# Kernel optimization log

Hardware: AMD Instinct MI355X
Metric: run time of the kernel (lower is better)

Reference implementation:

```python
import jax, jax.numpy as jnp
import numpy as np

N_NODES = 100000
N_EDGES = 1600000
DK = 32
OUT_DIM = 32


def setup_inputs() -> dict:
    key = jax.random.key(0)
    ks = jax.random.split(key, 7)
    X = jax.random.normal(ks[0], (N_NODES, DK), dtype=jnp.float32)
    K = jax.random.normal(ks[1], (N_NODES, DK), dtype=jnp.float32)
    V = jax.random.normal(ks[2], (N_NODES, DK), dtype=jnp.float32)
    # output projection (nn.Dense(out_dim)) params
    W_o = jax.random.normal(ks[3], (DK, OUT_DIM), dtype=jnp.float32) / np.sqrt(DK)
    b_o = jnp.zeros((OUT_DIM,), dtype=jnp.float32)
    # sparsity descriptor td: edge list, dst sorted so segment ops see sorted ids
    src = jax.random.randint(ks[4], (N_EDGES,), 0, N_NODES, dtype=jnp.int32)
    dst = jnp.sort(jax.random.randint(ks[5], (N_EDGES,), 0, N_NODES, dtype=jnp.int32))
    return {"X": X, "K": K, "V": V, "W_o": W_o, "b_o": b_o,
            "src": src, "dst": dst, "num_seg": N_NODES}


def reference(X, K, V, W_o, b_o, src, dst, num_seg):
    dk = X.shape[-1]
    # per-edge attention logits: <Q[dst], K[src]> / dk  -> (E,)
    scores = jnp.einsum('ed,ed->e', jnp.take(X, dst, axis=0),
                        jnp.take(K, src, axis=0)) / dk
    # segment (per-neighborhood) softmax over edges sharing a dst node
    seg_max = jax.ops.segment_max(scores, dst, num_segments=num_seg,
                                  indices_are_sorted=True)
    e = jnp.exp(scores - jnp.take(seg_max, dst))
    denom = jax.ops.segment_sum(e, dst, num_segments=num_seg,
                                indices_are_sorted=True)
    alpha = e / jnp.take(denom, dst)  # (E,)
    # weighted aggregation of values, scattered back to nodes -> (N, dk)
    agg = jax.ops.segment_sum(alpha[:, None] * jnp.take(V, src, axis=0), dst,
                              num_segments=num_seg, indices_are_sorted=True)
    # output projection W_o
    return agg @ W_o + b_o
```

## Files before the change

### kernel.cpp

```cpp
#include <hip/hip_runtime.h>
#include <math.h>

#define DK 32
#define OUT_DIM 32

typedef float    f32x4 __attribute__((ext_vector_type(4)));
typedef _Float16 h2    __attribute__((ext_vector_type(2)));
typedef _Float16 h8    __attribute__((ext_vector_type(8)));

#if __has_builtin(__builtin_amdgcn_fdot2)
#define FDOT2(a, b, c) __builtin_amdgcn_fdot2((a), (b), (c), false)
#else
#define FDOT2(a, b, c) ((c) + (float)(a).x * (float)(b).x + (float)(a).y * (float)(b).y)
#endif

__device__ __forceinline__ h2 as_h2(unsigned u) {
    union { unsigned u; h2 h; } v; v.u = u; return v.h;
}
__device__ __forceinline__ unsigned as_u32(h2 h) {
    union { unsigned u; h2 h; } v; v.h = h; return v.u;
}
__device__ __forceinline__ h2 shfl_xor_h2(h2 v, int m) {
    union { unsigned u; h2 h; } x; x.h = v;
    x.u = (unsigned)__shfl_xor((int)x.u, m);
    return x.h;
}

__global__ void prep_kernel(const int* __restrict__ dst,
                            const float4* __restrict__ K4,
                            const float4* __restrict__ V4,
                            int E, int N,
                            int* __restrict__ row_ptr,
                            uint4* __restrict__ KVH) {
    const int t = blockIdx.x * blockDim.x + threadIdx.x;
    if (t < E) {
        const int cur  = dst[t];
        const int prev = (t == 0) ? -1 : dst[t - 1];
        for (int j = prev + 1; j <= cur; ++j) row_ptr[j] = t;
        if (t == E - 1) {
            for (int j = cur + 1; j <= N; ++j) row_ptr[j] = E;
        }
    }
    if (t < N * 8) {
        const float4 kf = K4[t];
        const float4 vf = V4[t];
        h2 k01, k23, v01, v23;
        k01.x = (_Float16)kf.x;  k01.y = (_Float16)kf.y;
        k23.x = (_Float16)kf.z;  k23.y = (_Float16)kf.w;
        v01.x = (_Float16)vf.x;  v01.y = (_Float16)vf.y;
        v23.x = (_Float16)vf.z;  v23.y = (_Float16)vf.w;
        uint4 o;
        o.x = as_u32(k01); o.y = as_u32(k23); o.z = as_u32(v01); o.w = as_u32(v23);
        KVH[t] = o;
    }
}

__global__ void build_row_ptr_kernel(const int* __restrict__ dst, int E, int N,
                                     int* __restrict__ row_ptr) {
    int e = blockIdx.x * blockDim.x + threadIdx.x;
    if (e >= E) return;
    int cur  = dst[e];
    int prev = (e == 0) ? -1 : dst[e - 1];
    for (int j = prev + 1; j <= cur; ++j) row_ptr[j] = e;
    if (e == E - 1) {
        for (int j = cur + 1; j <= N; ++j) row_ptr[j] = E;
    }
}

__global__ __launch_bounds__(256) void gat_fused_kernel(
    const float* __restrict__ X, const uint4* __restrict__ KV,
    const float* __restrict__ Wo, const float* __restrict__ bo,
    const int* __restrict__ src, const int* __restrict__ row_ptr,
    float* __restrict__ out, int N) {

    __shared__ uint4 s_part[16 * 17];

    const int tid  = threadIdx.x;
    const int w    = tid >> 6;
    const int lane = tid & 63;
    const int g    = lane >> 3;
    const int c    = lane & 7;

    const int n_blk = blockIdx.x * 16;
    const int n_w   = n_blk + w * 4;

    const int rpv = row_ptr[min(n_w + min(lane, 4), N)];

    const float4* X4 = (const float4*)X;
    unsigned* part32 = (unsigned*)s_part;
    const float scale = 0.03125f;

    for (int pr = 0; pr < 2; ++pr) {
        const int ia = pr * 2;
        const int beginA = __builtin_amdgcn_readlane(rpv, ia);
        const int endA   = __builtin_amdgcn_readlane(rpv, ia + 1);
        const int endB   = __builtin_amdgcn_readlane(rpv, ia + 2);
        const int beginB = endA;
        const int nA = n_w + ia;
        const int nB = nA + 1;

        float4 qa = X4[min(nA, N - 1) * 8 + c];
        float4 qb = X4[min(nB, N - 1) * 8 + c];
        h2 qa01, qa23, qb01, qb23;
        qa01.x = (_Float16)(qa.x * scale);  qa01.y = (_Float16)(qa.y * scale);
        qa23.x = (_Float16)(qa.z * scale);  qa23.y = (_Float16)(qa.w * scale);
        qb01.x = (_Float16)(qb.x * scale);  qb01.y = (_Float16)(qb.y * scale);
        qb23.x = (_Float16)(qb.z * scale);  qb23.y = (_Float16)(qb.w * scale);

        float lA = 0.0f, lB = 0.0f;
        h2 aA01 = (h2)0, aA23 = (h2)0, aB01 = (h2)0, aB23 = (h2)0;

        const int capA = max(endA - 1, 0);
        const int capB = max(endB - 1, 0);
        int eA = beginA, eB = beginB;

        auto step = [&](const uint4& A0, const uint4& A1,
                        const uint4& B0, const uint4& B1) {
            float p0 = FDOT2(as_h2(A0.y), qa23, FDOT2(as_h2(A0.x), qa01, 0.0f));
            float p1 = FDOT2(as_h2(A1.y), qa23, FDOT2(as_h2(A1.x), qa01, 0.0f));
            float p2 = FDOT2(as_h2(B0.y), qb23, FDOT2(as_h2(B0.x), qb01, 0.0f));
            float p3 = FDOT2(as_h2(B1.y), qb23, FDOT2(as_h2(B1.x), qb01, 0.0f));
            p0 += __shfl_xor(p0, 1);  p1 += __shfl_xor(p1, 1);
            p2 += __shfl_xor(p2, 1);  p3 += __shfl_xor(p3, 1);
            p0 += __shfl_xor(p0, 2);  p1 += __shfl_xor(p1, 2);
            p2 += __shfl_xor(p2, 2);  p3 += __shfl_xor(p3, 2);
            p0 += __shfl_xor(p0, 4);  p1 += __shfl_xor(p1, 4);
            p2 += __shfl_xor(p2, 4);  p3 += __shfl_xor(p3, 4);

            const float w0 = (eA + g     < endA) ? __expf(p0) : 0.0f;
            const float w1 = (eA + 8 + g < endA) ? __expf(p1) : 0.0f;
            const float w2 = (eB + g     < endB) ? __expf(p2) : 0.0f;
            const float w3 = (eB + 8 + g < endB) ? __expf(p3) : 0.0f;
            lA += w0 + w1;
            lB += w2 + w3;

            h2 wh0; wh0.x = (_Float16)w0; wh0.y = wh0.x;
            h2 wh1; wh1.x = (_Float16)w1; wh1.y = wh1.x;
            h2 wh2; wh2.x = (_Float16)w2; wh2.y = wh2.x;
            h2 wh3; wh3.x = (_Float16)w3; wh3.y = wh3.x;
            aA01 += wh0 * as_h2(A0.z);  aA23 += wh0 * as_h2(A0.w);
            aA01 += wh1 * as_h2(A1.z);  aA23 += wh1 * as_h2(A1.w);
            aB01 += wh2 * as_h2(B0.z);  aB23 += wh2 * as_h2(B0.w);
            aB01 += wh3 * as_h2(B1.z);  aB23 += wh3 * as_h2(B1.w);
        };

        if (eA < endA || eB < endB) {
            int sp0 = src[min(eA + g,     capA)];
            int sp1 = src[min(eA + 8 + g, capA)];
            int sp2 = src[min(eB + g,     capB)];
            int sp3 = src[min(eB + 8 + g, capB)];
            uint4 P0 = KV[sp0 * 8 + c];
            uint4 P1 = KV[sp1 * 8 + c];
            uint4 P2 = KV[sp2 * 8 + c];
            uint4 P3 = KV[sp3 * 8 + c];
            int sq0 = 0, sq1 = 0, sq2 = 0, sq3 = 0;
            uint4 Q0, Q1, Q2, Q3;
            bool more = (eA + 16 < endA) || (eB + 16 < endB);
            if (more) {
                sq0 = src[min(eA + 16 + g, capA)];
                sq1 = src[min(eA + 24 + g, capA)];
                sq2 = src[min(eB + 16 + g, capB)];
                sq3 = src[min(eB + 24 + g, capB)];
            }
            for (;;) {
                bool more2 = false;
                if (more) {
                    Q0 = KV[sq0 * 8 + c];
                    Q1 = KV[sq1 * 8 + c];
                    Q2 = KV[sq2 * 8 + c];
                    Q3 = KV[sq3 * 8 + c];
                    more2 = (eA + 32 < endA) || (eB + 32 < endB);
                    if (more2) {
                        sp0 = src[min(eA + 32 + g, capA)];
                        sp1 = src[min(eA + 40 + g, capA)];
                        sp2 = src[min(eB + 32 + g, capB)];
                        sp3 = src[min(eB + 40 + g, capB)];
                    }
                }
                step(P0, P1, P2, P3);
                eA += 16; eB += 16;
                if (!more) break;

                bool more3 = false;
                if (more2) {
                    P0 = KV[sp0 * 8 + c];
                    P1 = KV[sp1 * 8 + c];
                    P2 = KV[sp2 * 8 + c];
                    P3 = KV[sp3 * 8 + c];
                    more3 = (eA + 32 < endA) || (eB + 32 < endB);
                    if (more3) {
                        sq0 = src[min(eA + 32 + g, capA)];
                        sq1 = src[min(eA + 40 + g, capA)];
                        sq2 = src[min(eB + 32 + g, capB)];
                        sq3 = src[min(eB + 40 + g, capB)];
                    }
                }
                step(Q0, Q1, Q2, Q3);
                eA += 16; eB += 16;
                if (!more2) break;
                more = more3;
            }
        }

        lA   += __shfl_xor(lA, 8);
        aA01 += shfl_xor_h2(aA01, 8);
        aA23 += shfl_xor_h2(aA23, 8);
        lA += __shfl_xor(lA, 16);  lA += __shfl_xor(lA, 32);

        lB   += __shfl_xor(lB, 8);
        aB01 += shfl_xor_h2(aB01, 8);
        aB23 += shfl_xor_h2(aB23, 8);
        lB += __shfl_xor(lB, 16);  lB += __shfl_xor(lB, 32);

        const float invA = (endA > beginA) ? (1.0f / lA) : 0.0f;
        const float invB = (endB > beginB) ? (1.0f / lB) : 0.0f;
        h2 ivA; ivA.x = (_Float16)invA; ivA.y = ivA.x;
        h2 ivB; ivB.x = (_Float16)invB; ivB.y = ivB.x;
        aA01 *= ivA;  aA23 *= ivA;
        aB01 *= ivB;  aB23 *= ivB;

        if ((g & 1) == 0) {
            const int p   = g >> 1;
            const int row = w * 4 + ia;
            int off = row * 68 + p * 16 + c * 2;
            part32[off]     = as_u32(aA01);
            part32[off + 1] = as_u32(aA23);
            off += 68;
            part32[off]     = as_u32(aB01);
            part32[off + 1] = as_u32(aB23);
        }
    }

    __syncthreads();

    if (w == 0) {
        const int quad = lane >> 4;
        const int col  = lane & 15;

        union BF { h8 v; _Float16 u[8]; };
        BF bf0, bf1;
#pragma unroll
        for (int j2 = 0; j2 < 8; ++j2) {
            bf0.u[j2] = (_Float16)Wo[(quad * 8 + j2) * OUT_DIM + col];
            bf1.u[j2] = (_Float16)Wo[(quad * 8 + j2) * OUT_DIM + 16 + col];
        }
        const float bias0 = bo[col];
        const float bias1 = bo[16 + col];

        union AF { uint4 u; h8 v; };
        f32x4 C0 = {bias0, bias0, bias0, bias0};
        f32x4 C1 = {bias1, bias1, bias1, bias1};
#pragma unroll
        for (int cc = 0; cc < 4; ++cc) {
            AF a;
            a.u = s_part[col * 17 + cc * 4 + quad];
            C0 = __builtin_amdgcn_mfma_f32_16x16x32_f16(a.v, bf0.v, C0, 0, 0, 0);
            C1 = __builtin_amdgcn_mfma_f32_16x16x32_f16(a.v, bf1.v, C1, 0, 0, 0);
        }
#pragma unroll
        for (int r = 0; r < 4; ++r) {
            const int n = n_blk + quad * 4 + r;
            if (n < N) {
                out[n * OUT_DIM + col]      = C0[r];
                out[n * OUT_DIM + 16 + col] = C1[r];
            }
        }
    }
}

__global__ __launch_bounds__(256) void gat_node_f32_kernel(
    const float* __restrict__ X, const float* __restrict__ Km,
    const float* __restrict__ Vm, const float* __restrict__ Wo,
    const float* __restrict__ bo, const int* __restrict__ src,
    const int* __restrict__ row_ptr, float* __restrict__ out, int N) {
    const int tid  = threadIdx.x;
    const int wave = tid >> 6;
    const int lane = tid & 63;
    const int g    = lane >> 3;
    const int c    = lane & 7;
    const int j    = lane & 31;
    const int half = lane >> 5;
    const int n = blockIdx.x * 4 + wave;
    if (n >= N) return;
    const int begin = row_ptr[n];
    const int end   = row_ptr[n + 1];
    const float4* X4 = (const float4*)X;
    const float4* K4 = (const float4*)Km;
    const float4* V4 = (const float4*)Vm;
    const float4 q4 = X4[n * 8 + c];
    float  l   = 0.0f;
    float4 acc = make_float4(0.0f, 0.0f, 0.0f, 0.0f);
    for (int e0 = begin; e0 < end; e0 += 16) {
        const int  ea = e0 + g;
        const int  eb = ea + 8;
        const bool va = ea < end;
        const bool vb = eb < end;
        const int sa = src[min(ea, end - 1)];
        const int sb = src[min(eb, end - 1)];
        const float4 ka  = K4[sa * 8 + c];
        const float4 kb  = K4[sb * 8 + c];
        const float4 vva = V4[sa * 8 + c];
        const float4 vvb = V4[sb * 8 + c];
        float pa = fmaf(ka.x, q4.x, fmaf(ka.y, q4.y, fmaf(ka.z, q4.z, ka.w * q4.w)));
        float pb = fmaf(kb.x, q4.x, fmaf(kb.y, q4.y, fmaf(kb.z, q4.z, kb.w * q4.w)));
        pa += __shfl_xor(pa, 1);  pb += __shfl_xor(pb, 1);
        pa += __shfl_xor(pa, 2);  pb += __shfl_xor(pb, 2);
        pa += __shfl_xor(pa, 4);  pb += __shfl_xor(pb, 4);
        const float wa = va ? __expf(pa * 0.03125f) : 0.0f;
        const float wb = vb ? __expf(pb * 0.03125f) : 0.0f;
        l += wa + wb;
        acc.x = fmaf(wa, vva.x, acc.x);  acc.y = fmaf(wa, vva.y, acc.y);
        acc.z = fmaf(wa, vva.z, acc.z);  acc.w = fmaf(wa, vva.w, acc.w);
        acc.x = fmaf(wb, vvb.x, acc.x);  acc.y = fmaf(wb, vvb.y, acc.y);
        acc.z = fmaf(wb, vvb.z, acc.z);  acc.w = fmaf(wb, vvb.w, acc.w);
    }
#pragma unroll
    for (int m = 8; m <= 32; m <<= 1) {
        l     += __shfl_xor(l, m);
        acc.x += __shfl_xor(acc.x, m);
        acc.y += __shfl_xor(acc.y, m);
        acc.z += __shfl_xor(acc.z, m);
        acc.w += __shfl_xor(acc.w, m);
    }
    const float inv = (end > begin) ? (1.0f / l) : 0.0f;
    float ag[4] = {acc.x, acc.y, acc.z, acc.w};
    float s = 0.0f;
#pragma unroll
    for (int k = 0; k < 32; ++k) {
        const float a = __int_as_float(
            __builtin_amdgcn_readlane(__float_as_int(ag[k & 3]), k >> 2));
        s = fmaf(a, Wo[k * OUT_DIM + j], s);
    }
    if (half == 0) {
        out[n * OUT_DIM + j] = fmaf(s, inv, bo[j]);
    }
}

extern "C" void kernel_launch(void* const* d_in, const int* in_sizes, int n_in,
                              void* d_out, int out_size, void* d_ws, size_t ws_size,
                              hipStream_t stream) {
    const float* X  = (const float*)d_in[0];
    const float* Km = (const float*)d_in[1];
    const float* Vm = (const float*)d_in[2];
    const float* Wo = (const float*)d_in[3];
    const float* bo = (const float*)d_in[4];
    const int* src  = (const int*)d_in[5];
    const int* dst  = (const int*)d_in[6];

    const int N = in_sizes[0] / DK;
    const int E = in_sizes[5];

    int* row_ptr = (int*)d_ws;
    const size_t kv_off = (((size_t)(N + 1) * 4) + 127) & ~(size_t)127;
    unsigned* KV = (unsigned*)((char*)d_ws + kv_off);
    const size_t need = kv_off + (size_t)N * DK * 4;
    float* out = (float*)d_out;

    const int tb = 256;

    if (ws_size >= need) {
        const int total  = N * 8;
        const int prep_n = (E > total) ? E : total;
        prep_kernel<<<(prep_n + tb - 1) / tb, tb, 0, stream>>>(
            dst, (const float4*)Km, (const float4*)Vm, E, N,
            row_ptr, (uint4*)KV);
        const int grid = (N + 15) / 16;
        gat_fused_kernel<<<grid, 256, 0, stream>>>(X, (const uint4*)KV, Wo, bo,
                                                   src, row_ptr, out, N);
    } else {
        build_row_ptr_kernel<<<(E + tb - 1) / tb, tb, 0, stream>>>(dst, E, N, row_ptr);
        const int grid = (N + 3) / 4;
        gat_node_f32_kernel<<<grid, 256, 0, stream>>>(X, Km, Vm, Wo, bo,
                                                      src, row_ptr, out, N);
    }
}
```

Measured before the change: 133.1 us.

## Process four nodes per wave concurrently with triple-buffered gather pipeline and exp2

The fused attention kernel now handles all four nodes of a wave in one pass instead of two pairs. Each node gets one 8-edge slot per step, and KV gathers run through a three-deep software pipeline so more loads are in flight. The 1/ln2 factor is folded into the query scale so the softmax weight is computed with a native exp2 instead of expf. The prep kernel now loads four dst entries per thread with an int4 read, which shrinks the grid that builds row_ptr. The price is higher register pressure from the four-way state and triple buffers, and the prep change adds a serial loop per thread.

```diff
diff --git a/kernel.cpp b/kernel.cpp
--- a/kernel.cpp
+++ b/kernel.cpp
@@ -12,6 +12,12 @@
 #define FDOT2(a, b, c) __builtin_amdgcn_fdot2((a), (b), (c), false)
 #else
 #define FDOT2(a, b, c) ((c) + (float)(a).x * (float)(b).x + (float)(a).y * (float)(b).y)
+#endif
+
+#if __has_builtin(__builtin_amdgcn_exp2f)
+#define EXP2F(x) __builtin_amdgcn_exp2f(x)
+#else
+#define EXP2F(x) exp2f(x)
 #endif
 
 __device__ __forceinline__ h2 as_h2(unsigned u) {
@@ -32,13 +38,28 @@
                             int E, int N,
                             int* __restrict__ row_ptr,
                             uint4* __restrict__ KVH) {
-    const int t = blockIdx.x * blockDim.x + threadIdx.x;
-    if (t < E) {
-        const int cur  = dst[t];
-        const int prev = (t == 0) ? -1 : dst[t - 1];
-        for (int j = prev + 1; j <= cur; ++j) row_ptr[j] = t;
-        if (t == E - 1) {
-            for (int j = cur + 1; j <= N; ++j) row_ptr[j] = E;
+    const int t  = blockIdx.x * blockDim.x + threadIdx.x;
+    const int e0 = t * 4;
+    if (e0 < E) {
+        int cur[4];
+        if (e0 + 4 <= E) {
+            const int4 dd = *(const int4*)(dst + e0);
+            cur[0] = dd.x; cur[1] = dd.y; cur[2] = dd.z; cur[3] = dd.w;
+        } else {
+#pragma unroll
+            for (int k = 0; k < 4; ++k)
+                cur[k] = (e0 + k < E) ? dst[e0 + k] : 0;
+        }
+        int prev = (e0 == 0) ? -1 : dst[e0 - 1];
+#pragma unroll
+        for (int k = 0; k < 4; ++k) {
+            const int ee = e0 + k;
+            if (ee < E) {
+                for (int j = prev + 1; j <= cur[k]; ++j) row_ptr[j] = ee;
+                if (ee == E - 1)
+                    for (int j = cur[k] + 1; j <= N; ++j) row_ptr[j] = E;
+                prev = cur[k];
+            }
         }
     }
     if (t < N * 8) {
@@ -88,146 +109,118 @@
 
     const float4* X4 = (const float4*)X;
     unsigned* part32 = (unsigned*)s_part;
-    const float scale = 0.03125f;
-
-    for (int pr = 0; pr < 2; ++pr) {
-        const int ia = pr * 2;
-        const int beginA = __builtin_amdgcn_readlane(rpv, ia);
-        const int endA   = __builtin_amdgcn_readlane(rpv, ia + 1);
-        const int endB   = __builtin_amdgcn_readlane(rpv, ia + 2);
-        const int beginB = endA;
-        const int nA = n_w + ia;
-        const int nB = nA + 1;
-
-        float4 qa = X4[min(nA, N - 1) * 8 + c];
-        float4 qb = X4[min(nB, N - 1) * 8 + c];
-        h2 qa01, qa23, qb01, qb23;
-        qa01.x = (_Float16)(qa.x * scale);  qa01.y = (_Float16)(qa.y * scale);
-        qa23.x = (_Float16)(qa.z * scale);  qa23.y = (_Float16)(qa.w * scale);
-        qb01.x = (_Float16)(qb.x * scale);  qb01.y = (_Float16)(qb.y * scale);
-        qb23.x = (_Float16)(qb.z * scale);  qb23.y = (_Float16)(qb.w * scale);
-
-        float lA = 0.0f, lB = 0.0f;
-        h2 aA01 = (h2)0, aA23 = (h2)0, aB01 = (h2)0, aB23 = (h2)0;
-
-        const int capA = max(endA - 1, 0);
-        const int capB = max(endB - 1, 0);
-        int eA = beginA, eB = beginB;
-
-        auto step = [&](const uint4& A0, const uint4& A1,
-                        const uint4& B0, const uint4& B1) {
-            float p0 = FDOT2(as_h2(A0.y), qa23, FDOT2(as_h2(A0.x), qa01, 0.0f));
-            float p1 = FDOT2(as_h2(A1.y), qa23, FDOT2(as_h2(A1.x), qa01, 0.0f));
-            float p2 = FDOT2(as_h2(B0.y), qb23, FDOT2(as_h2(B0.x), qb01, 0.0f));
-            float p3 = FDOT2(as_h2(B1.y), qb23, FDOT2(as_h2(B1.x), qb01, 0.0f));
-            p0 += __shfl_xor(p0, 1);  p1 += __shfl_xor(p1, 1);
-            p2 += __shfl_xor(p2, 1);  p3 += __shfl_xor(p3, 1);
-            p0 += __shfl_xor(p0, 2);  p1 += __shfl_xor(p1, 2);
-            p2 += __shfl_xor(p2, 2);  p3 += __shfl_xor(p3, 2);
-            p0 += __shfl_xor(p0, 4);  p1 += __shfl_xor(p1, 4);
-            p2 += __shfl_xor(p2, 4);  p3 += __shfl_xor(p3, 4);
-
-            const float w0 = (eA + g     < endA) ? __expf(p0) : 0.0f;
-            const float w1 = (eA + 8 + g < endA) ? __expf(p1) : 0.0f;
-            const float w2 = (eB + g     < endB) ? __expf(p2) : 0.0f;
-            const float w3 = (eB + 8 + g < endB) ? __expf(p3) : 0.0f;
-            lA += w0 + w1;
-            lB += w2 + w3;
-
-            h2 wh0; wh0.x = (_Float16)w0; wh0.y = wh0.x;
-            h2 wh1; wh1.x = (_Float16)w1; wh1.y = wh1.x;
-            h2 wh2; wh2.x = (_Float16)w2; wh2.y = wh2.x;
-            h2 wh3; wh3.x = (_Float16)w3; wh3.y = wh3.x;
-            aA01 += wh0 * as_h2(A0.z);  aA23 += wh0 * as_h2(A0.w);
-            aA01 += wh1 * as_h2(A1.z);  aA23 += wh1 * as_h2(A1.w);
-            aB01 += wh2 * as_h2(B0.z);  aB23 += wh2 * as_h2(B0.w);
-            aB01 += wh3 * as_h2(B1.z);  aB23 += wh3 * as_h2(B1.w);
-        };
-
-        if (eA < endA || eB < endB) {
-            int sp0 = src[min(eA + g,     capA)];
-            int sp1 = src[min(eA + 8 + g, capA)];
-            int sp2 = src[min(eB + g,     capB)];
-            int sp3 = src[min(eB + 8 + g, capB)];
-            uint4 P0 = KV[sp0 * 8 + c];
-            uint4 P1 = KV[sp1 * 8 + c];
-            uint4 P2 = KV[sp2 * 8 + c];
-            uint4 P3 = KV[sp3 * 8 + c];
-            int sq0 = 0, sq1 = 0, sq2 = 0, sq3 = 0;
-            uint4 Q0, Q1, Q2, Q3;
-            bool more = (eA + 16 < endA) || (eB + 16 < endB);
-            if (more) {
-                sq0 = src[min(eA + 16 + g, capA)];
-                sq1 = src[min(eA + 24 + g, capA)];
-                sq2 = src[min(eB + 16 + g, capB)];
-                sq3 = src[min(eB + 24 + g, capB)];
-            }
-            for (;;) {
-                bool more2 = false;
-                if (more) {
-                    Q0 = KV[sq0 * 8 + c];
-                    Q1 = KV[sq1 * 8 + c];
-                    Q2 = KV[sq2 * 8 + c];
-                    Q3 = KV[sq3 * 8 + c];
-                    more2 = (eA + 32 < endA) || (eB + 32 < endB);
-                    if (more2) {
-                        sp0 = src[min(eA + 32 + g, capA)];
-                        sp1 = src[min(eA + 40 + g, capA)];
-                        sp2 = src[min(eB + 32 + g, capB)];
-                        sp3 = src[min(eB + 40 + g, capB)];
-                    }
-                }
-                step(P0, P1, P2, P3);
-                eA += 16; eB += 16;
-                if (!more) break;
-
-                bool more3 = false;
-                if (more2) {
-                    P0 = KV[sp0 * 8 + c];
-                    P1 = KV[sp1 * 8 + c];
-                    P2 = KV[sp2 * 8 + c];
-                    P3 = KV[sp3 * 8 + c];
-                    more3 = (eA + 32 < endA) || (eB + 32 < endB);
-                    if (more3) {
-                        sq0 = src[min(eA + 32 + g, capA)];
-                        sq1 = src[min(eA + 40 + g, capA)];
-                        sq2 = src[min(eB + 32 + g, capB)];
-                        sq3 = src[min(eB + 40 + g, capB)];
-                    }
-                }
-                step(Q0, Q1, Q2, Q3);
-                eA += 16; eB += 16;
-                if (!more2) break;
-                more = more3;
-            }
-        }
-
-        lA   += __shfl_xor(lA, 8);
-        aA01 += shfl_xor_h2(aA01, 8);
-        aA23 += shfl_xor_h2(aA23, 8);
-        lA += __shfl_xor(lA, 16);  lA += __shfl_xor(lA, 32);
-
-        lB   += __shfl_xor(lB, 8);
-        aB01 += shfl_xor_h2(aB01, 8);
-        aB23 += shfl_xor_h2(aB23, 8);
-        lB += __shfl_xor(lB, 16);  lB += __shfl_xor(lB, 32);
-
-        const float invA = (endA > beginA) ? (1.0f / lA) : 0.0f;
-        const float invB = (endB > beginB) ? (1.0f / lB) : 0.0f;
-        h2 ivA; ivA.x = (_Float16)invA; ivA.y = ivA.x;
-        h2 ivB; ivB.x = (_Float16)invB; ivB.y = ivB.x;
-        aA01 *= ivA;  aA23 *= ivA;
-        aB01 *= ivB;  aB23 *= ivB;
-
-        if ((g & 1) == 0) {
-            const int p   = g >> 1;
-            const int row = w * 4 + ia;
-            int off = row * 68 + p * 16 + c * 2;
-            part32[off]     = as_u32(aA01);
-            part32[off + 1] = as_u32(aA23);
-            off += 68;
-            part32[off]     = as_u32(aB01);
-            part32[off + 1] = as_u32(aB23);
+    const float scale = 0.03125f * 1.44269504f;
+
+    int beg[4], en[4], cap[4], e[4];
+#pragma unroll
+    for (int i = 0; i < 4; ++i) {
+        beg[i] = __builtin_amdgcn_readlane(rpv, i);
+        en[i]  = __builtin_amdgcn_readlane(rpv, i + 1);
+        cap[i] = max(en[i] - 1, 0);
+        e[i]   = beg[i];
+    }
+
+    h2 q01[4], q23[4];
+#pragma unroll
+    for (int i = 0; i < 4; ++i) {
+        const float4 qf = X4[min(n_w + i, N - 1) * 8 + c];
+        q01[i].x = (_Float16)(qf.x * scale);
+        q01[i].y = (_Float16)(qf.y * scale);
+        q23[i].x = (_Float16)(qf.z * scale);
+        q23[i].y = (_Float16)(qf.w * scale);
+    }
+
+    float l[4] = {0.0f, 0.0f, 0.0f, 0.0f};
+    h2 a01[4], a23[4];
+#pragma unroll
+    for (int i = 0; i < 4; ++i) { a01[i] = (h2)0; a23[i] = (h2)0; }
+
+    auto ldsrc = [&](int o, int* s) {
+#pragma unroll
+        for (int i = 0; i < 4; ++i) s[i] = src[min(e[i] + o + g, cap[i])];
+    };
+    auto ldkv = [&](const int* s, uint4* B) {
+#pragma unroll
+        for (int i = 0; i < 4; ++i) B[i] = KV[s[i] * 8 + c];
+    };
+    auto step = [&](const uint4* B) {
+        float p[4];
+#pragma unroll
+        for (int i = 0; i < 4; ++i)
+            p[i] = FDOT2(as_h2(B[i].y), q23[i], FDOT2(as_h2(B[i].x), q01[i], 0.0f));
+#pragma unroll
+        for (int i = 0; i < 4; ++i) p[i] += __shfl_xor(p[i], 1);
+#pragma unroll
+        for (int i = 0; i < 4; ++i) p[i] += __shfl_xor(p[i], 2);
+#pragma unroll
+        for (int i = 0; i < 4; ++i) p[i] += __shfl_xor(p[i], 4);
+#pragma unroll
+        for (int i = 0; i < 4; ++i) {
+            const float wt = (e[i] + g < en[i]) ? EXP2F(p[i]) : 0.0f;
+            l[i] += wt;
+            h2 wh; wh.x = (_Float16)wt; wh.y = wh.x;
+            a01[i] += wh * as_h2(B[i].z);
+            a23[i] += wh * as_h2(B[i].w);
+        }
+    };
+    auto nexists = [&]() {
+        return (e[0] + 8 < en[0]) || (e[1] + 8 < en[1]) ||
+               (e[2] + 8 < en[2]) || (e[3] + 8 < en[3]);
+    };
+    auto adv = [&]() {
+#pragma unroll
+        for (int i = 0; i < 4; ++i) e[i] += 8;
+    };
+
+    const bool any0 = (e[0] < en[0]) || (e[1] < en[1]) ||
+                      (e[2] < en[2]) || (e[3] < en[3]);
+    if (any0) {
+        int s0[4], s1[4], s2[4], sCA[4], sAB[4], sBC[4];
+        uint4 B0[4], B1[4], B2[4];
+        ldsrc(0, s0);  ldsrc(8, s1);  ldsrc(16, s2);  ldsrc(24, sCA);
+        ldkv(s0, B0);  ldkv(s1, B1);  ldkv(s2, B2);
+
+        for (;;) {
+            bool mn = nexists();
+            step(B0);
+            ldkv(sCA, B0);
+            ldsrc(32, sAB);
+            adv();
+            if (!mn) break;
+            mn = nexists();
+            step(B1);
+            ldkv(sAB, B1);
+            ldsrc(32, sBC);
+            adv();
+            if (!mn) break;
+            mn = nexists();
+            step(B2);
+            ldkv(sBC, B2);
+            ldsrc(32, sCA);
+            adv();
+            if (!mn) break;
+        }
+    }
+
+#pragma unroll
+    for (int i = 0; i < 4; ++i) {
+        l[i]   += __shfl_xor(l[i], 8);
+        a01[i] += shfl_xor_h2(a01[i], 8);
+        a23[i] += shfl_xor_h2(a23[i], 8);
+        l[i] += __shfl_xor(l[i], 16);
+        l[i] += __shfl_xor(l[i], 32);
+        const float inv = (en[i] > beg[i]) ? (1.0f / l[i]) : 0.0f;
+        h2 iv; iv.x = (_Float16)inv; iv.y = iv.x;
+        a01[i] *= iv;  a23[i] *= iv;
+    }
+
+    if ((g & 1) == 0) {
+        const int p = g >> 1;
+#pragma unroll
+        for (int i = 0; i < 4; ++i) {
+            const int off = (w * 4 + i) * 68 + p * 16 + c * 2;
+            part32[off]     = as_u32(a01[i]);
+            part32[off + 1] = as_u32(a23[i]);
         }
     }
 
@@ -359,8 +352,9 @@
     const int tb = 256;
 
     if (ws_size >= need) {
-        const int total  = N * 8;
-        const int prep_n = (E > total) ? E : total;
+        const int nE4   = (E + 3) / 4;
+        const int total = N * 8;
+        const int prep_n = (nE4 > total) ? nE4 : total;
         prep_kernel<<<(prep_n + tb - 1) / tb, tb, 0, stream>>>(
             dst, (const float4*)Km, (const float4*)Vm, E, N,
             row_ptr, (uint4*)KV);
```

New measurement: 136.3 us. +2.4%, slower.
